# Kernel optimization log

Measured on AMD Instinct MI355X. Metric: run time of the kernel, lower is better.

The kernel has to match this reference:

```python
import jax, jax.numpy as jnp
import numpy as np

N_TASK = 50000
N_PROC = 256
N_EDGES = 800000
EMB = 64
HEADS = 4
NLAYERS = 3
EDIM = 8
TDIM = 16
PDIM = 8
NGRAPHS = 8


def setup_inputs():
    key = jax.random.key(0)
    ks = jax.random.split(key, 30)

    def nrm(k, shape, fan_in):
        return jax.random.normal(k, shape, jnp.float32) / np.float32(np.sqrt(fan_in))

    inp = {}
    inp["x_task"] = jax.random.normal(ks[0], (N_TASK, TDIM), jnp.float32)
    inp["x_proc"] = jax.random.normal(ks[1], (N_PROC, PDIM), jnp.float32)
    inp["edge_index"] = jax.random.randint(ks[2], (2, N_EDGES), 0, N_TASK, dtype=jnp.int32)
    inp["edge_attr"] = jax.random.uniform(ks[3], (N_EDGES, EDIM), jnp.float32)
    inp["task_batch"] = jnp.sort(jax.random.randint(ks[4], (N_TASK,), 0, NGRAPHS, dtype=jnp.int32))
    inp["proc_batch"] = jnp.sort(jax.random.randint(ks[5], (N_PROC,), 0, NGRAPHS, dtype=jnp.int32))
    # input embeds
    inp["W_task"] = nrm(ks[6], (TDIM, EMB), TDIM)
    inp["b_task"] = jnp.zeros((EMB,), jnp.float32)
    inp["W_proc"] = nrm(ks[7], (PDIM, EMB), PDIM)
    inp["b_proc"] = jnp.zeros((EMB,), jnp.float32)
    # per-layer GAT params (stacked over layers)
    inp["gat_W"] = nrm(ks[8], (NLAYERS, EMB, HEADS * EMB), EMB)
    inp["gat_We"] = nrm(ks[9], (NLAYERS, EDIM, HEADS * EMB), EDIM)
    inp["att_src"] = nrm(ks[10], (NLAYERS, HEADS, EMB), EMB)
    inp["att_dst"] = nrm(ks[11], (NLAYERS, HEADS, EMB), EMB)
    inp["att_edge"] = nrm(ks[12], (NLAYERS, HEADS, EMB), EMB)
    inp["gat_b"] = jnp.zeros((NLAYERS, HEADS * EMB), jnp.float32)
    inp["proj_W"] = nrm(ks[13], (NLAYERS, HEADS * EMB, EMB), HEADS * EMB)
    inp["proj_b"] = jnp.zeros((NLAYERS, EMB), jnp.float32)
    inp["ln_g"] = jnp.ones((NLAYERS, EMB), jnp.float32)
    inp["ln_b"] = jnp.zeros((NLAYERS, EMB), jnp.float32)
    # heads
    inp["pt_W1"] = nrm(ks[14], (EMB, EMB // 2), EMB)
    inp["pt_b1"] = jnp.zeros((EMB // 2,), jnp.float32)
    inp["pt_W2"] = nrm(ks[15], (EMB // 2, 1), EMB // 2)
    inp["pt_b2"] = jnp.zeros((1,), jnp.float32)
    inp["v_W1"] = nrm(ks[16], (2 * EMB, EMB), 2 * EMB)
    inp["v_b1"] = jnp.zeros((EMB,), jnp.float32)
    inp["v_W2"] = nrm(ks[17], (EMB, 1), EMB)
    inp["v_b2"] = jnp.zeros((1,), jnp.float32)
    return inp


def _gat_layer(x, src, dst, eattr, W, We, a_s, a_d, a_e, bias):
    # PyG GATConv(in=-1 shared lin, heads=H, concat=True, edge_dim) with self loops already appended
    n = x.shape[0]
    xl = (x @ W).reshape(n, HEADS, EMB)            # [N,H,D]
    el = (eattr @ We).reshape(-1, HEADS, EMB)      # [E,H,D]
    a_src = jnp.einsum("nhd,hd->nh", xl, a_s)
    a_dst = jnp.einsum("nhd,hd->nh", xl, a_d)
    a_edg = jnp.einsum("ehd,hd->eh", el, a_e)
    alpha = jax.nn.leaky_relu(a_src[src] + a_dst[dst] + a_edg, 0.2)  # [E,H]
    m = jax.ops.segment_max(alpha, dst, num_segments=n)
    ex = jnp.exp(alpha - m[dst])
    denom = jax.ops.segment_sum(ex, dst, num_segments=n)
    coeff = ex / (denom[dst] + 1e-16)
    out = jax.ops.segment_sum(coeff[:, :, None] * xl[src], dst, num_segments=n)
    return out.reshape(n, HEADS * EMB) + bias


def _mean_pool(x, batch, g):
    s = jax.ops.segment_sum(x, batch, num_segments=g)
    cnt = jax.ops.segment_sum(jnp.ones((x.shape[0], 1), x.dtype), batch, num_segments=g)
    return s / jnp.maximum(cnt, 1.0)


def reference(x_task, x_proc, edge_attr, W_task, b_task, W_proc, b_proc, gat_W, gat_We,
              att_src, att_dst, att_edge, gat_b, proj_W, proj_b, ln_g, ln_b,
              pt_W1, pt_b1, pt_W2, pt_b2, v_W1, v_b1, v_W2, v_b2,
              edge_index, task_batch, proc_batch):
    h_t = x_task @ W_task + b_task
    h_p = x_proc @ W_proc + b_proc
    # add self loops; self-loop edge_attr = mean of edge_attr (PyG fill_value='mean')
    loop = jnp.arange(N_TASK, dtype=edge_index.dtype)
    src = jnp.concatenate([edge_index[0], loop])
    dst = jnp.concatenate([edge_index[1], loop])
    ea = jnp.concatenate([edge_attr, jnp.broadcast_to(edge_attr.mean(0), (N_TASK, EDIM))], axis=0)
    for l in range(NLAYERS):
        upd = _gat_layer(h_t, src, dst, ea, gat_W[l], gat_We[l], att_src[l], att_dst[l], att_edge[l], gat_b[l])
        upd = jax.nn.elu(upd @ proj_W[l] + proj_b[l])
        h = h_t + upd
        mu = h.mean(-1, keepdims=True)
        var = ((h - mu) ** 2).mean(-1, keepdims=True)
        h_t = (h - mu) / jnp.sqrt(var + 1e-5) * ln_g[l] + ln_b[l]
    task_logits = (jax.nn.relu(h_t @ pt_W1 + pt_b1) @ pt_W2 + pt_b2)[:, 0]
    tp = _mean_pool(h_t, task_batch, NGRAPHS)
    pp = _mean_pool(h_p, proc_batch, NGRAPHS)
    ge = jnp.concatenate([tp, pp], axis=1)
    value = jax.nn.relu(ge @ v_W1 + v_b1) @ v_W2 + v_b2
    return task_logits, value, h_t, h_p
```

## Files before the change

### kernel.cpp

```cpp
#include <hip/hip_runtime.h>
#include <hip/hip_bf16.h>
#include <math.h>

#define NT 50000
#define NTP 50048
#define NP 256
#define NE 800000
#define ET 850000
#define EMBD 64
#define NHEADS 4
#define HE 256
#define NG 8

typedef __attribute__((ext_vector_type(8))) short bf16x8;
typedef __attribute__((ext_vector_type(4))) float f32x4;

#define OFF_DEG      0u
#define OFF_INDPTR   200192u
#define OFF_CURSOR   400384u
#define OFF_EIDS     600576u
#define OFF_SRCS     4000768u
#define OFF_MEAN     7400960u
#define OFF_M        7401216u
#define OFF_TPSUM    7401472u
#define OFF_TPCNT    7403520u
#define OFF_ASRC     7403776u
#define OFF_ADST     8204544u
#define OFF_SINV     9005312u
#define OFF_AEDG     9805568u
#define OFF_COEFF    23405568u
#define OFF_HT       37005568u
#define OFF_HTB      49817856u
#define OFF_XL       56224000u
#define OFF_AGG      81824000u
#define OFF_WXF      107448576u
#define OFF_WPF      107546880u

__device__ __forceinline__ float bf2f(unsigned short u) {
  union { unsigned int i; float f; } v; v.i = ((unsigned int)u) << 16; return v.f;
}
__device__ __forceinline__ float bf_lo(unsigned int u) {
  union { unsigned int i; float f; } v; v.i = u << 16; return v.f;
}
__device__ __forceinline__ float bf_hi(unsigned int u) {
  union { unsigned int i; float f; } v; v.i = u & 0xffff0000u; return v.f;
}

__global__ __launch_bounds__(256) void k_embed_task(const float* __restrict__ x,
    const float* __restrict__ W, const float* __restrict__ b,
    float* __restrict__ ht, __hip_bfloat16* __restrict__ htb) {
  int lane = threadIdx.x & 63, wid = threadIdx.x >> 6;
  float breg[16];
  #pragma unroll
  for (int k = 0; k < 16; k++) breg[k] = W[k * 64 + lane];
  float bias = b[lane];
  int row0 = blockIdx.x * 64 + wid * 16;
  #pragma unroll 1
  for (int r = 0; r < 16; r++) {
    int row = row0 + r;
    if (row >= NT) return;
    const float4* xr = (const float4*)(x + (size_t)row * 16);
    float acc = bias;
    #pragma unroll
    for (int q = 0; q < 4; q++) {
      float4 v = xr[q];
      acc += v.x * breg[q*4+0] + v.y * breg[q*4+1] + v.z * breg[q*4+2] + v.w * breg[q*4+3];
    }
    ht[(size_t)row * 64 + lane] = acc;
    htb[(size_t)row * 64 + lane] = __float2bfloat16(acc);
  }
}

__global__ __launch_bounds__(256) void k_embed_proc(const float* __restrict__ x,
    const float* __restrict__ W, const float* __restrict__ b, float* __restrict__ hp) {
  int lane = threadIdx.x & 63, wid = threadIdx.x >> 6;
  float breg[8];
  #pragma unroll
  for (int k = 0; k < 8; k++) breg[k] = W[k * 64 + lane];
  float bias = b[lane];
  #pragma unroll 1
  for (int r = 0; r < 64; r++) {
    int row = wid * 64 + r;
    const float* xr = x + (size_t)row * 8;
    float acc = bias;
    #pragma unroll
    for (int k = 0; k < 8; k++) acc += xr[k] * breg[k];
    hp[(size_t)row * 64 + lane] = acc;
  }
}

__global__ __launch_bounds__(256) void k_edge_mean(const float* __restrict__ ea,
                                                   float* __restrict__ sums) {
  __shared__ float lds[256];
  int k = threadIdx.x & 7;
  int rlane = threadIdx.x >> 3;
  float s = 0.f;
  for (int row = blockIdx.x * 32 + rlane; row < NE; row += gridDim.x * 32)
    s += ea[(size_t)row * 8 + k];
  lds[threadIdx.x] = s;
  __syncthreads();
  for (int off = 128; off >= 8; off >>= 1) {
    if (threadIdx.x < off) lds[threadIdx.x] += lds[threadIdx.x + off];
    __syncthreads();
  }
  if (threadIdx.x < 8) atomicAdd(&sums[threadIdx.x], lds[threadIdx.x]);
}

__global__ __launch_bounds__(256) void k_degree(const int* __restrict__ ei1, int* __restrict__ deg) {
  int e = blockIdx.x * 256 + threadIdx.x;
  if (e >= ET) return;
  int d = (e < NE) ? ei1[e] : (e - NE);
  atomicAdd(&deg[d], 1);
}

__global__ __launch_bounds__(1024) void k_scan(const int* __restrict__ deg, int* __restrict__ indptr) {
  __shared__ int wsum[16];
  __shared__ int carry;
  int tid = threadIdx.x, lane = tid & 63, wid = tid >> 6;
  if (tid == 0) carry = 0;
  __syncthreads();
  for (int base = 0; base < NT; base += 1024) {
    int i = base + tid;
    int v = (i < NT) ? deg[i] : 0;
    int x = v;
    #pragma unroll
    for (int off = 1; off < 64; off <<= 1) {
      int t = __shfl_up(x, off, 64);
      if (lane >= off) x += t;
    }
    if (lane == 63) wsum[wid] = x;
    __syncthreads();
    int c0 = carry;
    if (wid == 0 && lane < 16) {
      int w = wsum[lane];
      #pragma unroll
      for (int off = 1; off < 16; off <<= 1) {
        int t = __shfl_up(w, off, 64);
        if (lane >= off) w += t;
      }
      wsum[lane] = w;
    }
    __syncthreads();
    int woff = (wid == 0) ? 0 : wsum[wid - 1];
    int incl = x + woff;
    if (i < NT) indptr[i] = c0 + incl - v;
    __syncthreads();
    if (tid == 1023) carry = c0 + wsum[15];
    __syncthreads();
  }
  if (threadIdx.x == 0) indptr[NT] = carry;
}

__global__ __launch_bounds__(256) void k_copy(const int* __restrict__ a, int* __restrict__ b) {
  int i = blockIdx.x * 256 + threadIdx.x;
  if (i < NT) b[i] = a[i];
}

__global__ __launch_bounds__(256) void k_fill(const int* __restrict__ ei0,
                                              const int* __restrict__ ei1,
                                              int* __restrict__ cursor,
                                              int* __restrict__ eids,
                                              int* __restrict__ srcs) {
  int e = blockIdx.x * 256 + threadIdx.x;
  if (e >= ET) return;
  int d, s;
  if (e < NE) { d = ei1[e]; s = ei0[e]; } else { d = e - NE; s = e - NE; }
  int pos = atomicAdd(&cursor[d], 1);
  eids[pos] = e;
  srcs[pos] = s;
}

__global__ void k_prep_wx(const float* __restrict__ W, __hip_bfloat16* __restrict__ Wf) {
  int lane = threadIdx.x;
  int bid = blockIdx.x;
  int l = bid >> 5, rem = bid & 31, t = rem >> 1, kb = rem & 1;
  int quad = lane >> 4, l15 = lane & 15;
  const float* Wl = W + (size_t)l * 64 * 256;
  __hip_bfloat16* out = Wf + (size_t)l * 16384 + (size_t)((t * 2 + kb) * 64 + lane) * 8;
  #pragma unroll
  for (int j = 0; j < 8; j++)
    out[j] = __float2bfloat16(Wl[(kb * 32 + quad * 8 + j) * 256 + t * 16 + l15]);
}

__global__ void k_prep_wp(const float* __restrict__ W, __hip_bfloat16* __restrict__ Wf) {
  int lane = threadIdx.x;
  int bid = blockIdx.x;
  int l = bid >> 5, rem = bid & 31, t = rem >> 3, kb = rem & 7;
  int quad = lane >> 4, l15 = lane & 15;
  const float* Wl = W + (size_t)l * 256 * 64;
  __hip_bfloat16* out = Wf + (size_t)l * 16384 + (size_t)((t * 8 + kb) * 64 + lane) * 8;
  #pragma unroll
  for (int j = 0; j < 8; j++)
    out[j] = __float2bfloat16(Wl[(kb * 32 + quad * 8 + j) * 64 + t * 16 + l15]);
}

__global__ __launch_bounds__(256) void k_xl_mfma(
    const __hip_bfloat16* __restrict__ htb, const __hip_bfloat16* __restrict__ Wf,
    const float* __restrict__ as, const float* __restrict__ ad,
    __hip_bfloat16* __restrict__ xl, float* __restrict__ a_src, float* __restrict__ a_dst) {
  int lane = threadIdx.x & 63, wave = threadIdx.x >> 6;
  int quad = lane >> 4, l15 = lane & 15;
  int r0 = blockIdx.x * 64 + wave * 16;
  f32x4 acc[16];
  #pragma unroll
  for (int t = 0; t < 16; t++) acc[t] = (f32x4){0.f, 0.f, 0.f, 0.f};
  #pragma unroll
  for (int kb = 0; kb < 2; kb++) {
    bf16x8 a = *(const bf16x8*)(htb + (size_t)(r0 + l15) * 64 + kb * 32 + quad * 8);
    #pragma unroll
    for (int t = 0; t < 16; t++) {
      bf16x8 bfr = *(const bf16x8*)(Wf + (size_t)((t * 2 + kb) * 64 + lane) * 8);
      acc[t] = __builtin_amdgcn_mfma_f32_16x16x32_bf16(a, bfr, acc[t], 0, 0, 0);
    }
  }
  float asv[16], adv[16];
  #pragma unroll
  for (int t = 0; t < 16; t++) { asv[t] = as[t * 16 + l15]; adv[t] = ad[t * 16 + l15]; }
  #pragma unroll
  for (int reg = 0; reg < 4; reg++) {
    int row = r0 + quad * 4 + reg;
    bool ok = row < NT;
    float vs[4] = {0.f, 0.f, 0.f, 0.f}, vd[4] = {0.f, 0.f, 0.f, 0.f};
    #pragma unroll
    for (int t = 0; t < 16; t++) {
      float v = acc[t][reg];
      if (ok) xl[(size_t)row * HE + t * 16 + l15] = __float2bfloat16(v);
      vs[t >> 2] += v * asv[t];
      vd[t >> 2] += v * adv[t];
    }
    #pragma unroll
    for (int off = 8; off; off >>= 1) {
      #pragma unroll
      for (int h = 0; h < 4; h++) {
        vs[h] += __shfl_xor(vs[h], off, 64);
        vd[h] += __shfl_xor(vd[h], off, 64);
      }
    }
    if (ok && l15 == 0) {
      float4 s4; s4.x = vs[0]; s4.y = vs[1]; s4.z = vs[2]; s4.w = vs[3];
      float4 d4; d4.x = vd[0]; d4.y = vd[1]; d4.z = vd[2]; d4.w = vd[3];
      *(float4*)(a_src + (size_t)row * 4) = s4;
      *(float4*)(a_dst + (size_t)row * 4) = d4;
    }
  }
}

__global__ void k_att_edge_mat(const float* __restrict__ We, const float* __restrict__ ae,
                               float* __restrict__ M) {
  int t = threadIdx.x;
  if (t >= 32) return;
  int k = t >> 2, h = t & 3;
  float s = 0.f;
  for (int d = 0; d < 64; d++) s += We[k * HE + h * 64 + d] * ae[h * 64 + d];
  M[k * 4 + h] = s;
}

__global__ __launch_bounds__(256) void k_a_edg(const float* __restrict__ ea,
    const float* __restrict__ msum, const float* __restrict__ M, float* __restrict__ aedg) {
  int e = blockIdx.x * 256 + threadIdx.x;
  if (e >= ET) return;
  float v[8];
  if (e < NE) {
    const float4* p = (const float4*)(ea + (size_t)e * 8);
    float4 x0 = p[0], x1 = p[1];
    v[0] = x0.x; v[1] = x0.y; v[2] = x0.z; v[3] = x0.w;
    v[4] = x1.x; v[5] = x1.y; v[6] = x1.z; v[7] = x1.w;
  } else {
    #pragma unroll
    for (int k = 0; k < 8; k++) v[k] = msum[k] * (1.f / NE);
  }
  float rr[4];
  #pragma unroll
  for (int h = 0; h < 4; h++) {
    float s = 0.f;
    #pragma unroll
    for (int k = 0; k < 8; k++) s += v[k] * M[k * 4 + h];
    rr[h] = s;
  }
  float4 r; r.x = rr[0]; r.y = rr[1]; r.z = rr[2]; r.w = rr[3];
  *(float4*)(aedg + (size_t)e * 4) = r;
}

__global__ __launch_bounds__(256) void k_softmax(
    const float* __restrict__ a_src, const float* __restrict__ a_dst,
    const float* __restrict__ a_edg, const int* __restrict__ indptr,
    const int* __restrict__ eids, const int* __restrict__ srcs,
    float* __restrict__ coeff, float* __restrict__ sinv) {
  int node = blockIdx.x * 4 + (threadIdx.x >> 6);
  int lane = threadIdx.x & 63;
  int beg = indptr[node], end = indptr[node + 1];
  float4 ad = *(const float4*)(a_dst + (size_t)node * 4);
  float m[4] = {-1e30f, -1e30f, -1e30f, -1e30f};
  for (int i = beg + lane; i < end; i += 64) {
    int e = eids[i], s = srcs[i];
    float4 asr = *(const float4*)(a_src + (size_t)s * 4);
    float4 aer = *(const float4*)(a_edg + (size_t)e * 4);
    float al[4] = {asr.x + ad.x + aer.x, asr.y + ad.y + aer.y,
                   asr.z + ad.z + aer.z, asr.w + ad.w + aer.w};
    #pragma unroll
    for (int h = 0; h < 4; h++) {
      float a = al[h];
      a = (a > 0.f) ? a : 0.2f * a;
      al[h] = a;
      m[h] = fmaxf(m[h], a);
    }
    float4 c; c.x = al[0]; c.y = al[1]; c.z = al[2]; c.w = al[3];
    *(float4*)(coeff + (size_t)i * 4) = c;
  }
  #pragma unroll
  for (int off = 32; off; off >>= 1) {
    #pragma unroll
    for (int h = 0; h < 4; h++) m[h] = fmaxf(m[h], __shfl_xor(m[h], off, 64));
  }
  float sm[4] = {0.f, 0.f, 0.f, 0.f};
  for (int i = beg + lane; i < end; i += 64) {
    float4 al = *(const float4*)(coeff + (size_t)i * 4);
    float ex[4];
    ex[0] = __expf(al.x - m[0]);
    ex[1] = __expf(al.y - m[1]);
    ex[2] = __expf(al.z - m[2]);
    ex[3] = __expf(al.w - m[3]);
    #pragma unroll
    for (int h = 0; h < 4; h++) sm[h] += ex[h];
    float4 c; c.x = ex[0]; c.y = ex[1]; c.z = ex[2]; c.w = ex[3];
    *(float4*)(coeff + (size_t)i * 4) = c;
  }
  #pragma unroll
  for (int off = 32; off; off >>= 1) {
    #pragma unroll
    for (int h = 0; h < 4; h++) sm[h] += __shfl_xor(sm[h], off, 64);
  }
  if (lane == 0) {
    #pragma unroll
    for (int h = 0; h < 4; h++) sinv[node * 4 + h] = 1.f / (sm[h] + 1e-16f);
  }
}

__global__ __launch_bounds__(256) void k_aggregate(
    const __hip_bfloat16* __restrict__ xl, const float* __restrict__ coeff,
    const float* __restrict__ sinv, const int* __restrict__ indptr,
    const int* __restrict__ srcs, const float* __restrict__ gb,
    __hip_bfloat16* __restrict__ agg) {
  int node = blockIdx.x * 4 + (threadIdx.x >> 6);
  int lane = threadIdx.x & 63;
  int h = lane >> 4;
  int hbase = lane & 48;
  int beg = indptr[node], end = indptr[node + 1];
  float acc0 = 0.f, acc1 = 0.f, acc2 = 0.f, acc3 = 0.f;
  for (int base = beg; base < end; base += 64) {
    int cnt = min(64, end - base);
    int my_src = (lane < cnt) ? srcs[base + lane] : 0;
    for (int c16 = 0; c16 < cnt; c16 += 16) {
      int n16 = min(16, cnt - c16);
      int el = c16 + (lane & 15);
      float my_cf = (el < cnt) ? coeff[(size_t)(base + el) * 4 + h] : 0.f;
      if (n16 == 16) {
        #pragma unroll 4
        for (int j = 0; j < 16; j++) {
          int src = __shfl(my_src, c16 + j, 64);
          float cf = __shfl(my_cf, hbase | j, 64);
          uint2 u = *(const uint2*)(xl + (size_t)src * HE + lane * 4);
          acc0 += cf * bf_lo(u.x);
          acc1 += cf * bf_hi(u.x);
          acc2 += cf * bf_lo(u.y);
          acc3 += cf * bf_hi(u.y);
        }
      } else {
        for (int j = 0; j < n16; j++) {
          int src = __shfl(my_src, c16 + j, 64);
          float cf = __shfl(my_cf, hbase | j, 64);
          uint2 u = *(const uint2*)(xl + (size_t)src * HE + lane * 4);
          acc0 += cf * bf_lo(u.x);
          acc1 += cf * bf_hi(u.x);
          acc2 += cf * bf_lo(u.y);
          acc3 += cf * bf_hi(u.y);
        }
      }
    }
  }
  float inv = sinv[node * 4 + h];
  float4 g4 = *(const float4*)(gb + lane * 4);
  unsigned int o0 = __bfloat16_as_ushort(__float2bfloat16(acc0 * inv + g4.x));
  unsigned int o1 = __bfloat16_as_ushort(__float2bfloat16(acc1 * inv + g4.y));
  unsigned int o2 = __bfloat16_as_ushort(__float2bfloat16(acc2 * inv + g4.z));
  unsigned int o3 = __bfloat16_as_ushort(__float2bfloat16(acc3 * inv + g4.w));
  uint2 out; out.x = o0 | (o1 << 16); out.y = o2 | (o3 << 16);
  *(uint2*)(agg + (size_t)node * HE + lane * 4) = out;
}

__global__ __launch_bounds__(256) void k_proj_mfma(
    const __hip_bfloat16* __restrict__ agg, const __hip_bfloat16* __restrict__ Wf,
    const float* __restrict__ pb, const float* __restrict__ g, const float* __restrict__ b,
    const float* __restrict__ ht_in, float* __restrict__ ht_out,
    __hip_bfloat16* __restrict__ htb_out, int writebf) {
  int lane = threadIdx.x & 63, wave = threadIdx.x >> 6;
  int quad = lane >> 4, l15 = lane & 15;
  int r0 = blockIdx.x * 64 + wave * 16;
  f32x4 acc[4];
  #pragma unroll
  for (int t = 0; t < 4; t++) acc[t] = (f32x4){0.f, 0.f, 0.f, 0.f};
  #pragma unroll
  for (int kb = 0; kb < 8; kb++) {
    bf16x8 a = *(const bf16x8*)(agg + (size_t)(r0 + l15) * HE + kb * 32 + quad * 8);
    #pragma unroll
    for (int t = 0; t < 4; t++) {
      bf16x8 bfr = *(const bf16x8*)(Wf + (size_t)((t * 8 + kb) * 64 + lane) * 8);
      acc[t] = __builtin_amdgcn_mfma_f32_16x16x32_bf16(a, bfr, acc[t], 0, 0, 0);
    }
  }
  float pbv[4], gv[4], bv[4];
  #pragma unroll
  for (int t = 0; t < 4; t++) {
    pbv[t] = pb[t * 16 + l15];
    gv[t] = g[t * 16 + l15];
    bv[t] = b[t * 16 + l15];
  }
  #pragma unroll
  for (int reg = 0; reg < 4; reg++) {
    int row = r0 + quad * 4 + reg;
    bool ok = row < NT;
    float h[4], rs = 0.f;
    #pragma unroll
    for (int t = 0; t < 4; t++) {
      float u = acc[t][reg] + pbv[t];
      u = (u > 0.f) ? u : (__expf(u) - 1.f);
      h[t] = ht_in[(size_t)row * 64 + t * 16 + l15] + u;
      rs += h[t];
    }
    #pragma unroll
    for (int off = 8; off; off >>= 1) rs += __shfl_xor(rs, off, 64);
    float mu = rs * 0.015625f;
    float vv = 0.f;
    #pragma unroll
    for (int t = 0; t < 4; t++) { float d = h[t] - mu; vv += d * d; }
    #pragma unroll
    for (int off = 8; off; off >>= 1) vv += __shfl_xor(vv, off, 64);
    float rstd = rsqrtf(vv * 0.015625f + 1e-5f);
    #pragma unroll
    for (int t = 0; t < 4; t++) {
      float o = (h[t] - mu) * rstd * gv[t] + bv[t];
      if (ok) {
        ht_out[(size_t)row * 64 + t * 16 + l15] = o;
        if (writebf) htb_out[(size_t)row * 64 + t * 16 + l15] = __float2bfloat16(o);
      }
    }
  }
}

__global__ __launch_bounds__(256) void k_task_head(const float* __restrict__ ht,
    const float* __restrict__ W1, const float* __restrict__ b1,
    const float* __restrict__ W2, const float* __restrict__ b2, float* __restrict__ logits) {
  __shared__ float lh[8 * 64];
  int t = threadIdx.x;
  size_t base = (size_t)blockIdx.x * 8 * 64;
  lh[t] = ht[base + t];
  lh[t + 256] = ht[base + t + 256];
  __syncthreads();
  int i = t >> 5, j = t & 31;
  float s = b1[j];
  #pragma unroll 8
  for (int d = 0; d < 64; d++) s += lh[i * 64 + d] * W1[d * 32 + j];
  s = fmaxf(s, 0.f);
  float p = s * W2[j];
  #pragma unroll
  for (int off = 16; off; off >>= 1) p += __shfl_xor(p, off, 64);
  if (j == 0) logits[blockIdx.x * 8 + i] = p + b2[0];
}

__global__ __launch_bounds__(256) void k_pool_task(const float* __restrict__ ht,
    const int* __restrict__ tb, float* __restrict__ sums, float* __restrict__ cnt) {
  int lane = threadIdx.x & 63, sub = threadIdx.x >> 6;
  float acc[8], c[8];
  #pragma unroll
  for (int g = 0; g < 8; g++) { acc[g] = 0.f; c[g] = 0.f; }
  int lim = min(NT, (int)((blockIdx.x + 1) * 512));
  for (int n = blockIdx.x * 512 + sub; n < lim; n += 4) {
    int g = tb[n];
    float v = ht[(size_t)n * 64 + lane];
    #pragma unroll
    for (int gg = 0; gg < 8; gg++) {
      if (g == gg) { acc[gg] += v; c[gg] += 1.f; }
    }
  }
  #pragma unroll
  for (int g = 0; g < 8; g++) {
    if (__any(acc[g] != 0.f || c[g] != 0.f)) {
      atomicAdd(&sums[g * 64 + lane], acc[g]);
      if (lane == 0) atomicAdd(&cnt[g], c[g]);
    }
  }
}

__global__ __launch_bounds__(512) void k_value(const float* __restrict__ tpsum,
    const float* __restrict__ tpcnt, const float* __restrict__ hp,
    const int* __restrict__ pbatch, const float* __restrict__ vW1,
    const float* __restrict__ vb1, const float* __restrict__ vW2,
    const float* __restrict__ vb2, float* __restrict__ val_out) {
  __shared__ float ge[8 * 128];
  int t = threadIdx.x;
  int g = t >> 6, d = t & 63;
  float c = fmaxf(tpcnt[g], 1.f);
  ge[g * 128 + d] = tpsum[g * 64 + d] / c;
  float s = 0.f, cc = 0.f;
  for (int p = 0; p < 256; p++) {
    int bg = pbatch[p];
    if (bg == g) { s += hp[(size_t)p * 64 + d]; cc += 1.f; }
  }
  ge[g * 128 + 64 + d] = s / fmaxf(cc, 1.f);
  __syncthreads();
  float acc = vb1[d];
  #pragma unroll 8
  for (int k = 0; k < 128; k++) acc += ge[g * 128 + k] * vW1[k * 64 + d];
  acc = fmaxf(acc, 0.f);
  float p = acc * vW2[d];
  #pragma unroll
  for (int off = 32; off; off >>= 1) p += __shfl_xor(p, off, 64);
  if (d == 0) val_out[g] = p + vb2[0];
}

extern "C" void kernel_launch(void* const* d_in, const int* in_sizes, int n_in,
                              void* d_out, int out_size, void* d_ws, size_t ws_size,
                              hipStream_t stream) {
  (void)in_sizes; (void)n_in; (void)out_size; (void)ws_size;
  const float* x_task  = (const float*)d_in[0];
  const float* x_proc  = (const float*)d_in[1];
  const int*   eidx    = (const int*)d_in[2];
  const float* eattr   = (const float*)d_in[3];
  const int*   tbatch  = (const int*)d_in[4];
  const int*   pbatch  = (const int*)d_in[5];
  const float* W_task  = (const float*)d_in[6];
  const float* b_task  = (const float*)d_in[7];
  const float* W_proc  = (const float*)d_in[8];
  const float* b_proc  = (const float*)d_in[9];
  const float* gat_W   = (const float*)d_in[10];
  const float* gat_We  = (const float*)d_in[11];
  const float* att_src = (const float*)d_in[12];
  const float* att_dst = (const float*)d_in[13];
  const float* att_edge= (const float*)d_in[14];
  const float* gat_b   = (const float*)d_in[15];
  const float* proj_W  = (const float*)d_in[16];
  const float* proj_b  = (const float*)d_in[17];
  const float* ln_g    = (const float*)d_in[18];
  const float* ln_b    = (const float*)d_in[19];
  const float* pt_W1   = (const float*)d_in[20];
  const float* pt_b1   = (const float*)d_in[21];
  const float* pt_W2   = (const float*)d_in[22];
  const float* pt_b2   = (const float*)d_in[23];
  const float* v_W1    = (const float*)d_in[24];
  const float* v_b1    = (const float*)d_in[25];
  const float* v_W2    = (const float*)d_in[26];
  const float* v_b2    = (const float*)d_in[27];

  char* ws = (char*)d_ws;
  int*   deg    = (int*)(ws + OFF_DEG);
  int*   indptr = (int*)(ws + OFF_INDPTR);
  int*   cursor = (int*)(ws + OFF_CURSOR);
  int*   eids   = (int*)(ws + OFF_EIDS);
  int*   srcs   = (int*)(ws + OFF_SRCS);
  float* msum   = (float*)(ws + OFF_MEAN);
  float* Mmat   = (float*)(ws + OFF_M);
  float* tpsum  = (float*)(ws + OFF_TPSUM);
  float* tpcnt  = (float*)(ws + OFF_TPCNT);
  float* a_src  = (float*)(ws + OFF_ASRC);
  float* a_dst  = (float*)(ws + OFF_ADST);
  float* sinv   = (float*)(ws + OFF_SINV);
  float* a_edg  = (float*)(ws + OFF_AEDG);
  float* coeff  = (float*)(ws + OFF_COEFF);
  float* ht     = (float*)(ws + OFF_HT);
  __hip_bfloat16* htb = (__hip_bfloat16*)(ws + OFF_HTB);
  __hip_bfloat16* xl  = (__hip_bfloat16*)(ws + OFF_XL);
  __hip_bfloat16* agg = (__hip_bfloat16*)(ws + OFF_AGG);
  __hip_bfloat16* wxf = (__hip_bfloat16*)(ws + OFF_WXF);
  __hip_bfloat16* wpf = (__hip_bfloat16*)(ws + OFF_WPF);

  float* out_logits = (float*)d_out;
  float* out_value  = (float*)d_out + NT;
  float* out_ht     = (float*)d_out + NT + NG;
  float* out_hp     = (float*)d_out + NT + NG + (size_t)NT * EMBD;

  hipMemsetAsync(ws + OFF_DEG, 0, NT * 4, stream);
  hipMemsetAsync(ws + OFF_MEAN, 0, 2816, stream);

  k_embed_task<<<782, 256, 0, stream>>>(x_task, W_task, b_task, ht, htb);
  k_embed_proc<<<1, 256, 0, stream>>>(x_proc, W_proc, b_proc, out_hp);
  k_edge_mean<<<256, 256, 0, stream>>>(eattr, msum);
  k_degree<<<(ET + 255) / 256, 256, 0, stream>>>(eidx + NE, deg);
  k_scan<<<1, 1024, 0, stream>>>(deg, indptr);
  k_copy<<<(NT + 255) / 256, 256, 0, stream>>>(indptr, cursor);
  k_fill<<<(ET + 255) / 256, 256, 0, stream>>>(eidx, eidx + NE, cursor, eids, srcs);
  k_prep_wx<<<96, 64, 0, stream>>>(gat_W, wxf);
  k_prep_wp<<<96, 64, 0, stream>>>(proj_W, wpf);

  for (int l = 0; l < 3; l++) {
    k_xl_mfma<<<782, 256, 0, stream>>>(htb, wxf + (size_t)l * 16384,
                                       att_src + l * NHEADS * EMBD,
                                       att_dst + l * NHEADS * EMBD,
                                       xl, a_src, a_dst);
    k_att_edge_mat<<<1, 32, 0, stream>>>(gat_We + (size_t)l * 8 * HE,
                                         att_edge + l * NHEADS * EMBD, Mmat);
    k_a_edg<<<(ET + 255) / 256, 256, 0, stream>>>(eattr, msum, Mmat, a_edg);
    k_softmax<<<NT / 4, 256, 0, stream>>>(a_src, a_dst, a_edg, indptr, eids, srcs,
                                          coeff, sinv);
    k_aggregate<<<NT / 4, 256, 0, stream>>>(xl, coeff, sinv, indptr, srcs,
                                            gat_b + l * HE, agg);
    float* htout = (l == 2) ? out_ht : ht;
    k_proj_mfma<<<782, 256, 0, stream>>>(agg, wpf + (size_t)l * 16384,
                                         proj_b + l * EMBD, ln_g + l * EMBD,
                                         ln_b + l * EMBD, ht, htout, htb,
                                         (l == 2) ? 0 : 1);
  }

  k_task_head<<<NT / 8, 256, 0, stream>>>(out_ht, pt_W1, pt_b1, pt_W2, pt_b2, out_logits);
  k_pool_task<<<(NT + 511) / 512, 256, 0, stream>>>(out_ht, tbatch, tpsum, tpcnt);
  k_value<<<1, 512, 0, stream>>>(tpsum, tpcnt, out_hp, pbatch, v_W1, v_b1, v_W2, v_b2, out_value);
}
```

Measured before the change: 806.8 us.

## Fuse edge softmax into aggregation with online softmax and CSR-ordered edge logits

Replaces the separate softmax and aggregate kernels with one kernel that computes leaky-relu attention logits per 16-edge chunk and keeps a running max and sum, as in online softmax. This removes the coeff buffer round trip and the eids indirection. Edge attention terms are now scattered straight into CSR order through a per-edge position array, and the tiny edge-matrix kernel is folded into k_a_edg. The cursor copy is merged into the scan. In exchange, each block recomputes the small 8x4 matrix and the scatter writes become uncoalesced.

```diff
diff --git a/kernel.cpp b/kernel.cpp
--- a/kernel.cpp
+++ b/kernel.cpp
@@ -3,7 +3,6 @@
 #include <math.h>
 
 #define NT 50000
-#define NTP 50048
 #define NP 256
 #define NE 800000
 #define ET 850000
@@ -18,7 +17,7 @@
 #define OFF_DEG      0u
 #define OFF_INDPTR   200192u
 #define OFF_CURSOR   400384u
-#define OFF_EIDS     600576u
+#define OFF_POS      600576u
 #define OFF_SRCS     4000768u
 #define OFF_MEAN     7400960u
 #define OFF_M        7401216u
@@ -26,9 +25,7 @@
 #define OFF_TPCNT    7403520u
 #define OFF_ASRC     7403776u
 #define OFF_ADST     8204544u
-#define OFF_SINV     9005312u
 #define OFF_AEDG     9805568u
-#define OFF_COEFF    23405568u
 #define OFF_HT       37005568u
 #define OFF_HTB      49817856u
 #define OFF_XL       56224000u
@@ -36,9 +33,6 @@
 #define OFF_WXF      107448576u
 #define OFF_WPF      107546880u
 
-__device__ __forceinline__ float bf2f(unsigned short u) {
-  union { unsigned int i; float f; } v; v.i = ((unsigned int)u) << 16; return v.f;
-}
 __device__ __forceinline__ float bf_lo(unsigned int u) {
   union { unsigned int i; float f; } v; v.i = u << 16; return v.f;
 }
@@ -113,7 +107,9 @@
   atomicAdd(&deg[d], 1);
 }
 
-__global__ __launch_bounds__(1024) void k_scan(const int* __restrict__ deg, int* __restrict__ indptr) {
+__global__ __launch_bounds__(1024) void k_scan(const int* __restrict__ deg,
+                                               int* __restrict__ indptr,
+                                               int* __restrict__ cursor) {
   __shared__ int wsum[16];
   __shared__ int carry;
   int tid = threadIdx.x, lane = tid & 63, wid = tid >> 6;
@@ -143,7 +139,11 @@
     __syncthreads();
     int woff = (wid == 0) ? 0 : wsum[wid - 1];
     int incl = x + woff;
-    if (i < NT) indptr[i] = c0 + incl - v;
+    if (i < NT) {
+      int excl = c0 + incl - v;
+      indptr[i] = excl;
+      cursor[i] = excl;
+    }
     __syncthreads();
     if (tid == 1023) carry = c0 + wsum[15];
     __syncthreads();
@@ -151,23 +151,18 @@
   if (threadIdx.x == 0) indptr[NT] = carry;
 }
 
-__global__ __launch_bounds__(256) void k_copy(const int* __restrict__ a, int* __restrict__ b) {
-  int i = blockIdx.x * 256 + threadIdx.x;
-  if (i < NT) b[i] = a[i];
-}
-
 __global__ __launch_bounds__(256) void k_fill(const int* __restrict__ ei0,
                                               const int* __restrict__ ei1,
                                               int* __restrict__ cursor,
-                                              int* __restrict__ eids,
+                                              int* __restrict__ pos,
                                               int* __restrict__ srcs) {
   int e = blockIdx.x * 256 + threadIdx.x;
   if (e >= ET) return;
   int d, s;
   if (e < NE) { d = ei1[e]; s = ei0[e]; } else { d = e - NE; s = e - NE; }
-  int pos = atomicAdd(&cursor[d], 1);
-  eids[pos] = e;
-  srcs[pos] = s;
+  int p = atomicAdd(&cursor[d], 1);
+  srcs[p] = s;
+  pos[e] = p;
 }
 
 __global__ void k_prep_wx(const float* __restrict__ W, __hip_bfloat16* __restrict__ Wf) {
@@ -245,19 +240,21 @@
   }
 }
 
-__global__ void k_att_edge_mat(const float* __restrict__ We, const float* __restrict__ ae,
-                               float* __restrict__ M) {
+__global__ __launch_bounds__(256) void k_a_edg(const float* __restrict__ ea,
+    const float* __restrict__ msum, const float* __restrict__ We,
+    const float* __restrict__ ae, const int* __restrict__ pos,
+    float* __restrict__ aedg_csr) {
+  __shared__ float Ms[32];
   int t = threadIdx.x;
-  if (t >= 32) return;
-  int k = t >> 2, h = t & 3;
-  float s = 0.f;
-  for (int d = 0; d < 64; d++) s += We[k * HE + h * 64 + d] * ae[h * 64 + d];
-  M[k * 4 + h] = s;
-}
-
-__global__ __launch_bounds__(256) void k_a_edg(const float* __restrict__ ea,
-    const float* __restrict__ msum, const float* __restrict__ M, float* __restrict__ aedg) {
-  int e = blockIdx.x * 256 + threadIdx.x;
+  if (t < 32) {
+    int k = t >> 2, hh = t & 3;
+    float s = 0.f;
+    #pragma unroll
+    for (int d = 0; d < 64; d++) s += We[k * HE + hh * 64 + d] * ae[hh * 64 + d];
+    Ms[t] = s;
+  }
+  __syncthreads();
+  int e = blockIdx.x * 256 + t;
   if (e >= ET) return;
   float v[8];
   if (e < NE) {
@@ -274,111 +271,73 @@
   for (int h = 0; h < 4; h++) {
     float s = 0.f;
     #pragma unroll
-    for (int k = 0; k < 8; k++) s += v[k] * M[k * 4 + h];
+    for (int k = 0; k < 8; k++) s += v[k] * Ms[k * 4 + h];
     rr[h] = s;
   }
   float4 r; r.x = rr[0]; r.y = rr[1]; r.z = rr[2]; r.w = rr[3];
-  *(float4*)(aedg + (size_t)e * 4) = r;
-}
-
-__global__ __launch_bounds__(256) void k_softmax(
-    const float* __restrict__ a_src, const float* __restrict__ a_dst,
-    const float* __restrict__ a_edg, const int* __restrict__ indptr,
-    const int* __restrict__ eids, const int* __restrict__ srcs,
-    float* __restrict__ coeff, float* __restrict__ sinv) {
-  int node = blockIdx.x * 4 + (threadIdx.x >> 6);
-  int lane = threadIdx.x & 63;
-  int beg = indptr[node], end = indptr[node + 1];
-  float4 ad = *(const float4*)(a_dst + (size_t)node * 4);
-  float m[4] = {-1e30f, -1e30f, -1e30f, -1e30f};
-  for (int i = beg + lane; i < end; i += 64) {
-    int e = eids[i], s = srcs[i];
-    float4 asr = *(const float4*)(a_src + (size_t)s * 4);
-    float4 aer = *(const float4*)(a_edg + (size_t)e * 4);
-    float al[4] = {asr.x + ad.x + aer.x, asr.y + ad.y + aer.y,
-                   asr.z + ad.z + aer.z, asr.w + ad.w + aer.w};
-    #pragma unroll
-    for (int h = 0; h < 4; h++) {
-      float a = al[h];
-      a = (a > 0.f) ? a : 0.2f * a;
-      al[h] = a;
-      m[h] = fmaxf(m[h], a);
-    }
-    float4 c; c.x = al[0]; c.y = al[1]; c.z = al[2]; c.w = al[3];
-    *(float4*)(coeff + (size_t)i * 4) = c;
-  }
-  #pragma unroll
-  for (int off = 32; off; off >>= 1) {
-    #pragma unroll
-    for (int h = 0; h < 4; h++) m[h] = fmaxf(m[h], __shfl_xor(m[h], off, 64));
-  }
-  float sm[4] = {0.f, 0.f, 0.f, 0.f};
-  for (int i = beg + lane; i < end; i += 64) {
-    float4 al = *(const float4*)(coeff + (size_t)i * 4);
-    float ex[4];
-    ex[0] = __expf(al.x - m[0]);
-    ex[1] = __expf(al.y - m[1]);
-    ex[2] = __expf(al.z - m[2]);
-    ex[3] = __expf(al.w - m[3]);
-    #pragma unroll
-    for (int h = 0; h < 4; h++) sm[h] += ex[h];
-    float4 c; c.x = ex[0]; c.y = ex[1]; c.z = ex[2]; c.w = ex[3];
-    *(float4*)(coeff + (size_t)i * 4) = c;
-  }
-  #pragma unroll
-  for (int off = 32; off; off >>= 1) {
-    #pragma unroll
-    for (int h = 0; h < 4; h++) sm[h] += __shfl_xor(sm[h], off, 64);
-  }
-  if (lane == 0) {
-    #pragma unroll
-    for (int h = 0; h < 4; h++) sinv[node * 4 + h] = 1.f / (sm[h] + 1e-16f);
-  }
-}
-
-__global__ __launch_bounds__(256) void k_aggregate(
-    const __hip_bfloat16* __restrict__ xl, const float* __restrict__ coeff,
-    const float* __restrict__ sinv, const int* __restrict__ indptr,
-    const int* __restrict__ srcs, const float* __restrict__ gb,
-    __hip_bfloat16* __restrict__ agg) {
+  *(float4*)(aedg_csr + (size_t)pos[e] * 4) = r;
+}
+
+__global__ __launch_bounds__(256) void k_attn(
+    const __hip_bfloat16* __restrict__ xl, const float* __restrict__ a_src,
+    const float* __restrict__ a_dst, const float* __restrict__ aedg_csr,
+    const int* __restrict__ indptr, const int* __restrict__ srcs,
+    const float* __restrict__ gb, __hip_bfloat16* __restrict__ agg) {
   int node = blockIdx.x * 4 + (threadIdx.x >> 6);
   int lane = threadIdx.x & 63;
   int h = lane >> 4;
   int hbase = lane & 48;
+  int e15 = lane & 15;
   int beg = indptr[node], end = indptr[node + 1];
+  float adh = a_dst[node * 4 + h];
+  float M = -1e30f, S = 0.f;
   float acc0 = 0.f, acc1 = 0.f, acc2 = 0.f, acc3 = 0.f;
-  for (int base = beg; base < end; base += 64) {
-    int cnt = min(64, end - base);
-    int my_src = (lane < cnt) ? srcs[base + lane] : 0;
-    for (int c16 = 0; c16 < cnt; c16 += 16) {
-      int n16 = min(16, cnt - c16);
-      int el = c16 + (lane & 15);
-      float my_cf = (el < cnt) ? coeff[(size_t)(base + el) * 4 + h] : 0.f;
-      if (n16 == 16) {
-        #pragma unroll 4
-        for (int j = 0; j < 16; j++) {
-          int src = __shfl(my_src, c16 + j, 64);
-          float cf = __shfl(my_cf, hbase | j, 64);
-          uint2 u = *(const uint2*)(xl + (size_t)src * HE + lane * 4);
-          acc0 += cf * bf_lo(u.x);
-          acc1 += cf * bf_hi(u.x);
-          acc2 += cf * bf_lo(u.y);
-          acc3 += cf * bf_hi(u.y);
-        }
-      } else {
-        for (int j = 0; j < n16; j++) {
-          int src = __shfl(my_src, c16 + j, 64);
-          float cf = __shfl(my_cf, hbase | j, 64);
-          uint2 u = *(const uint2*)(xl + (size_t)src * HE + lane * 4);
-          acc0 += cf * bf_lo(u.x);
-          acc1 += cf * bf_hi(u.x);
-          acc2 += cf * bf_lo(u.y);
-          acc3 += cf * bf_hi(u.y);
-        }
+  for (int base = beg; base < end; base += 16) {
+    int cnt = min(16, end - base);
+    int el = base + e15;
+    bool ok = e15 < cnt;
+    int my_src = ok ? srcs[el] : 0;
+    float aer = ok ? aedg_csr[(size_t)el * 4 + h] : 0.f;
+    float asr = ok ? a_src[(size_t)my_src * 4 + h] : 0.f;
+    float al = asr + adh + aer;
+    al = (al > 0.f) ? al : 0.2f * al;
+    if (!ok) al = -1e30f;
+    float cm = al;
+    #pragma unroll
+    for (int off = 1; off < 16; off <<= 1) cm = fmaxf(cm, __shfl_xor(cm, off, 64));
+    float newM = fmaxf(M, cm);
+    float corr = __expf(M - newM);
+    float ex = __expf(al - newM);
+    float cs = ex;
+    #pragma unroll
+    for (int off = 1; off < 16; off <<= 1) cs += __shfl_xor(cs, off, 64);
+    S = S * corr + cs;
+    M = newM;
+    acc0 *= corr; acc1 *= corr; acc2 *= corr; acc3 *= corr;
+    if (cnt == 16) {
+      #pragma unroll 4
+      for (int j = 0; j < 16; j++) {
+        int src = __shfl(my_src, j, 64);
+        float cf = __shfl(ex, hbase | j, 64);
+        uint2 u = *(const uint2*)(xl + (size_t)src * HE + lane * 4);
+        acc0 += cf * bf_lo(u.x);
+        acc1 += cf * bf_hi(u.x);
+        acc2 += cf * bf_lo(u.y);
+        acc3 += cf * bf_hi(u.y);
       }
-    }
-  }
-  float inv = sinv[node * 4 + h];
+    } else {
+      for (int j = 0; j < cnt; j++) {
+        int src = __shfl(my_src, j, 64);
+        float cf = __shfl(ex, hbase | j, 64);
+        uint2 u = *(const uint2*)(xl + (size_t)src * HE + lane * 4);
+        acc0 += cf * bf_lo(u.x);
+        acc1 += cf * bf_hi(u.x);
+        acc2 += cf * bf_lo(u.y);
+        acc3 += cf * bf_hi(u.y);
+      }
+    }
+  }
+  float inv = 1.f / (S + 1e-16f);
   float4 g4 = *(const float4*)(gb + lane * 4);
   unsigned int o0 = __bfloat16_as_ushort(__float2bfloat16(acc0 * inv + g4.x));
   unsigned int o1 = __bfloat16_as_ushort(__float2bfloat16(acc1 * inv + g4.y));
@@ -555,17 +514,14 @@
   int*   deg    = (int*)(ws + OFF_DEG);
   int*   indptr = (int*)(ws + OFF_INDPTR);
   int*   cursor = (int*)(ws + OFF_CURSOR);
-  int*   eids   = (int*)(ws + OFF_EIDS);
+  int*   pos    = (int*)(ws + OFF_POS);
   int*   srcs   = (int*)(ws + OFF_SRCS);
   float* msum   = (float*)(ws + OFF_MEAN);
-  float* Mmat   = (float*)(ws + OFF_M);
   float* tpsum  = (float*)(ws + OFF_TPSUM);
   float* tpcnt  = (float*)(ws + OFF_TPCNT);
   float* a_src  = (float*)(ws + OFF_ASRC);
   float* a_dst  = (float*)(ws + OFF_ADST);
-  float* sinv   = (float*)(ws + OFF_SINV);
   float* a_edg  = (float*)(ws + OFF_AEDG);
-  float* coeff  = (float*)(ws + OFF_COEFF);
   float* ht     = (float*)(ws + OFF_HT);
   __hip_bfloat16* htb = (__hip_bfloat16*)(ws + OFF_HTB);
   __hip_bfloat16* xl  = (__hip_bfloat16*)(ws + OFF_XL);
@@ -585,9 +541,8 @@
   k_embed_proc<<<1, 256, 0, stream>>>(x_proc, W_proc, b_proc, out_hp);
   k_edge_mean<<<256, 256, 0, stream>>>(eattr, msum);
   k_degree<<<(ET + 255) / 256, 256, 0, stream>>>(eidx + NE, deg);
-  k_scan<<<1, 1024, 0, stream>>>(deg, indptr);
-  k_copy<<<(NT + 255) / 256, 256, 0, stream>>>(indptr, cursor);
-  k_fill<<<(ET + 255) / 256, 256, 0, stream>>>(eidx, eidx + NE, cursor, eids, srcs);
+  k_scan<<<1, 1024, 0, stream>>>(deg, indptr, cursor);
+  k_fill<<<(ET + 255) / 256, 256, 0, stream>>>(eidx, eidx + NE, cursor, pos, srcs);
   k_prep_wx<<<96, 64, 0, stream>>>(gat_W, wxf);
   k_prep_wp<<<96, 64, 0, stream>>>(proj_W, wpf);
 
@@ -596,13 +551,12 @@
                                        att_src + l * NHEADS * EMBD,
                                        att_dst + l * NHEADS * EMBD,
                                        xl, a_src, a_dst);
-    k_att_edge_mat<<<1, 32, 0, stream>>>(gat_We + (size_t)l * 8 * HE,
-                                         att_edge + l * NHEADS * EMBD, Mmat);
-    k_a_edg<<<(ET + 255) / 256, 256, 0, stream>>>(eattr, msum, Mmat, a_edg);
-    k_softmax<<<NT / 4, 256, 0, stream>>>(a_src, a_dst, a_edg, indptr, eids, srcs,
-                                          coeff, sinv);
-    k_aggregate<<<NT / 4, 256, 0, stream>>>(xl, coeff, sinv, indptr, srcs,
-                                            gat_b + l * HE, agg);
+    k_a_edg<<<(ET + 255) / 256, 256, 0, stream>>>(eattr, msum,
+                                                  gat_We + (size_t)l * 8 * HE,
+                                                  att_edge + l * NHEADS * EMBD,
+                                                  pos, a_edg);
+    k_attn<<<NT / 4, 256, 0, stream>>>(xl, a_src, a_dst, a_edg, indptr, srcs,
+                                       gat_b + l * HE, agg);
     float* htout = (l == 2) ? out_ht : ht;
     k_proj_mfma<<<782, 256, 0, stream>>>(agg, wpf + (size_t)l * 16384,
                                          proj_b + l * EMBD, ln_g + l * EMBD,
```

Result: faster. 768.6 us (-4.7%).
